# Kernel optimization log

Hardware: AMD Instinct MI355X
Metric: run time of the kernel (lower is better)

## Reference

```python
import jax, jax.numpy as jnp
import numpy as np

N_NODES = 100000
N_EDGES = 1600000
F_IN = 128
HID = 128
N_GRAPHS = 64


def setup_inputs() -> dict:
    key = jax.random.key(0)
    ks = jax.random.split(key, 12)
    x = jax.random.normal(ks[0], (N_NODES, F_IN), dtype=jnp.float32)
    edge_index = jax.random.randint(ks[1], (2, N_EDGES), 0, N_NODES, dtype=jnp.int32)
    batch = jnp.sort(jax.random.randint(ks[2], (N_NODES,), 0, N_GRAPHS, dtype=jnp.int32))
    s = 1.0 / np.sqrt(F_IN)
    W1 = jax.random.normal(ks[3], (F_IN, HID), dtype=jnp.float32) * s
    b1 = jnp.zeros((HID,), jnp.float32)
    W2 = jax.random.normal(ks[4], (HID, HID), dtype=jnp.float32) * s
    b2 = jnp.zeros((HID,), jnp.float32)
    W3 = jax.random.normal(ks[5], (HID, HID), dtype=jnp.float32) * s
    b3 = jnp.zeros((HID,), jnp.float32)
    Wc1 = jax.random.normal(ks[6], (HID, HID // 2), dtype=jnp.float32) * s
    bc1 = jnp.zeros((HID // 2,), jnp.float32)
    Wc2 = jax.random.normal(ks[7], (HID // 2, 1), dtype=jnp.float32) * (1.0 / np.sqrt(HID // 2))
    bc2 = jnp.zeros((1,), jnp.float32)
    return {"x": x, "edge_index": edge_index, "batch": batch,
            "W1": W1, "b1": b1, "W2": W2, "b2": b2, "W3": W3, "b3": b3,
            "Wc1": Wc1, "bc1": bc1, "Wc2": Wc2, "bc2": bc2}


def _gcn_conv(x, W, b, src, dst, norm, n_nodes):
    # PyG GCNConv: x' = D^-1/2 (A+I) D^-1/2 (x W) + b  (self-loops already in src/dst)
    h = x @ W                                   # [N, H] small GEMM
    msg = h[src] * norm[:, None]                # [E+N, H] gather (memory bound)
    out = jax.ops.segment_sum(msg, dst, num_segments=n_nodes)  # scatter-add
    return out + b


def reference(x, edge_index, batch, W1, b1, W2, b2, W3, b3, Wc1, bc1, Wc2, bc2):
    n = x.shape[0]
    loop = jnp.arange(n, dtype=edge_index.dtype)
    src = jnp.concatenate([edge_index[0], loop])
    dst = jnp.concatenate([edge_index[1], loop])
    deg = jax.ops.segment_sum(jnp.ones_like(dst, dtype=x.dtype), dst, num_segments=n)
    dinv = jax.lax.rsqrt(jnp.maximum(deg, 1.0))
    norm = dinv[src] * dinv[dst]                # [E+N]

    h = jax.nn.elu(_gcn_conv(x, W1, b1, src, dst, norm, n))   # dropout is identity in eval
    h = jax.nn.elu(_gcn_conv(h, W2, b2, src, dst, norm, n))
    h = jax.nn.elu(_gcn_conv(h, W3, b3, src, dst, norm, n))

    # global mean pool over graphs
    sums = jax.ops.segment_sum(h, batch, num_segments=N_GRAPHS)
    cnts = jax.ops.segment_sum(jnp.ones((n,), h.dtype), batch, num_segments=N_GRAPHS)
    g = sums / jnp.maximum(cnts, 1.0)[:, None]  # [G, H]

    z = jax.nn.relu(g @ Wc1 + bc1)
    logits = z @ Wc2 + bc2
    return jax.nn.sigmoid(logits)               # [G, 1]
```

## Files before the change

kernel.cpp:

```cpp
#include <hip/hip_runtime.h>
#include <cstdint>
#include <cstddef>


#define SUBCAP 512
#define CSRCAP 4608
#define TILE 4096

typedef __attribute__((ext_vector_type(8))) short short8;
typedef __attribute__((ext_vector_type(4))) float f32x4;
typedef __attribute__((ext_vector_type(2))) _Float16 h16x2;

__device__ __forceinline__ float bf2f(uint32_t u) {
  return __uint_as_float(u << 16);
}
__device__ __forceinline__ uint32_t f2bf(float f) {
  uint32_t x = __float_as_uint(f);
  return (x + 0x7FFFu + ((x >> 16) & 1u)) >> 16;
}

union H16 { _Float16 h; uint16_t u; };
union H2U { h16x2 h; uint32_t u; };

__device__ __forceinline__ uint32_t f2e5m2(float f) {
  f = fminf(fmaxf(f, -30000.f), 30000.f);
  H16 cv;
  cv.h = (_Float16)f;
  uint32_t h = cv.u;
  uint32_t r = h + 0x7Fu + ((h >> 8) & 1u);
  return (r >> 8) & 0xFFu;
}

__device__ __forceinline__ float e5m2f(uint32_t b) {
  H16 cv;
  cv.u = (uint16_t)(b << 8);
  return (float)cv.h;
}


__global__ __launch_bounds__(256) void bucket_scatter(const int* __restrict__ src,
                                                      const int* __restrict__ dst,
                                                      int* __restrict__ bcur,
                                                      uint32_t* __restrict__ ebuf,
                                                      int nE, int nbuk) {
  uint32_t xcc;
  asm("s_getreg_b32 %0, hwreg(HW_REG_XCC_ID)" : "=s"(xcc));
  __shared__ int lhist[1024];
  __shared__ int gbase[1024];
  int t = threadIdx.x;
  for (int i = t; i < nbuk; i += 256) lhist[i] = 0;
  __syncthreads();

  int e0 = blockIdx.x * TILE;
  int myd[16], mys[16], myrank[16];
#pragma unroll
  for (int j = 0; j < 16; ++j) {
    int e = e0 + t + j * 256;
    if (e < nE) {
      int d = dst[e];
      myd[j] = d;
      mys[j] = src[e];
      myrank[j] = atomicAdd(&lhist[d >> 7], 1);
    } else {
      myd[j] = -1;
    }
  }
  __syncthreads();
  for (int i = t; i < nbuk; i += 256) {
    int c = lhist[i];
    gbase[i] = c ? atomicAdd(&bcur[((i << 3) | (int)xcc) * 16], c) : 0;
  }
  __syncthreads();
#pragma unroll
  for (int j = 0; j < 16; ++j) {
    if (myd[j] >= 0) {
      int b = myd[j] >> 7;
      int pos = gbase[b] + myrank[j];
      if (pos < SUBCAP) {
        int sub = (b << 3) | (int)xcc;
        ebuf[(size_t)sub * SUBCAP + pos] =
            ((uint32_t)(myd[j] & 127) << 20) | (uint32_t)mys[j];
      }
    }
  }
}

__global__ __launch_bounds__(256) void bucket_build(const uint32_t* __restrict__ ebuf,
                                                    const int* __restrict__ bcur,
                                                    int* __restrict__ deg,
                                                    float* __restrict__ dinv,
                                                    int* __restrict__ offs,
                                                    int* __restrict__ csr,
                                                    const float* __restrict__ W1,
                                                    const float* __restrict__ W2,
                                                    const float* __restrict__ W3,
                                                    uint16_t* __restrict__ WT,
                                                    float* __restrict__ pool,
                                                    int n, int nbuk) {
  int b = blockIdx.x;
  int base = b << 7;
  __shared__ int hist[128];
  __shared__ int pre[128];
  __shared__ int lcur[128];
  int t = threadIdx.x;

  for (int id = b * 256 + t; id < 3 * 16384; id += nbuk * 256) {
    int w = id >> 14;
    int rem = id & 16383;
    int k = rem >> 7, nn = rem & 127;
    const float* W = (w == 0) ? W1 : ((w == 1) ? W2 : W3);
    WT[w * 16384 + nn * 128 + k] = (uint16_t)f2bf(W[k * 128 + nn]);
  }
  for (int id = b * 256 + t; id < 64 * 128; id += nbuk * 256) pool[id] = 0.f;

  if (t < 128) hist[t] = 0;
  __syncthreads();
  int cnts[8];
#pragma unroll
  for (int x = 0; x < 8; ++x) {
    int sub = (b << 3) | x;
    int cnt = min(bcur[sub * 16], SUBCAP);
    cnts[x] = cnt;
    const uint32_t* eb = ebuf + (size_t)sub * SUBCAP;
    for (int e = t; e < cnt; e += 256) atomicAdd(&hist[eb[e] >> 20], 1);
  }
  __syncthreads();
  if (t < 128) pre[t] = (hist[t] + 3) & ~3;
  __syncthreads();
  for (int d = 1; d < 128; d <<= 1) {
    int v = (t >= d && t < 128) ? pre[t - d] : 0;
    __syncthreads();
    if (t < 128) pre[t] += v;
    __syncthreads();
  }
  if (t < 128) {
    int dg = hist[t];
    int start = b * CSRCAP + pre[t] - ((dg + 3) & ~3);
    lcur[t] = start;
    if (base + t < n) {
      deg[base + t] = dg;
      dinv[base + t] = rsqrtf((float)(dg + 1));
      offs[base + t] = start;
    }
  }
  __syncthreads();
#pragma unroll
  for (int x = 0; x < 8; ++x) {
    int sub = (b << 3) | x;
    int cnt = cnts[x];
    const uint32_t* eb = ebuf + (size_t)sub * SUBCAP;
    for (int e = t; e < cnt; e += 256) {
      uint32_t ed = eb[e];
      int pos = atomicAdd(&lcur[ed >> 20], 1);
      csr[pos] = (int)((ed & 0xFFFFFu) << 7);
    }
  }
}


template <bool F32IN>
__global__ __launch_bounds__(256) void gemm_mfma(const uint16_t* __restrict__ Xb,
                                                 const float* __restrict__ X32,
                                                 const uint16_t* __restrict__ WTb,
                                                 const float* __restrict__ dinv,
                                                 uint8_t* __restrict__ tab, int n) {
  __shared__ uint16_t sW[128 * 136];
  int t = threadIdx.x;
#pragma unroll
  for (int i = 0; i < 8; ++i) {
    int j = t + i * 256;
    int r = j >> 4, c = j & 15;
    float4 v = ((const float4*)WTb)[j];
    *(float4*)(sW + r * 136 + c * 8) = v;
  }
  __syncthreads();

  int wave = t >> 6, lane = t & 63;
  int quad = lane >> 4, l15 = lane & 15;
  int m = blockIdx.x * 64 + wave * 16 + l15;
  int mm = min(m, n - 1);

  short8 a[4];
#pragma unroll
  for (int kc = 0; kc < 4; ++kc) {
    if constexpr (F32IN) {
      const float* p = X32 + (size_t)mm * 128 + kc * 32 + quad * 8;
      float4 lo = *(const float4*)p;
      float4 hi = *(const float4*)(p + 4);
      a[kc] = (short8){(short)f2bf(lo.x), (short)f2bf(lo.y),
                       (short)f2bf(lo.z), (short)f2bf(lo.w),
                       (short)f2bf(hi.x), (short)f2bf(hi.y),
                       (short)f2bf(hi.z), (short)f2bf(hi.w)};
    } else {
      a[kc] = *(const short8*)(Xb + (size_t)mm * 128 + kc * 32 + quad * 8);
    }
  }

  f32x4 acc[8];
#pragma unroll
  for (int nn = 0; nn < 8; ++nn) acc[nn] = (f32x4){0.f, 0.f, 0.f, 0.f};

#pragma unroll
  for (int nn = 0; nn < 8; ++nn) {
    int nrow = nn * 16 + l15;
#pragma unroll
    for (int kc = 0; kc < 4; ++kc) {
      short8 b = *(const short8*)(sW + nrow * 136 + kc * 32 + quad * 8);
      acc[nn] = __builtin_amdgcn_mfma_f32_16x16x32_bf16(a[kc], b, acc[nn], 0, 0, 0);
    }
  }

  int mrow = blockIdx.x * 64 + wave * 16 + quad * 4;
#pragma unroll
  for (int r = 0; r < 4; ++r) {
    int row = mrow + r;
    if (row < n) {
      float dn = dinv[row];
#pragma unroll
      for (int nn = 0; nn < 8; ++nn) {
        tab[(size_t)row * 128 + nn * 16 + l15] = (uint8_t)f2e5m2(acc[nn][r] * dn);
      }
    }
  }
}


__device__ __forceinline__ void acc_pk(uint32_t u, h16x2& a01, h16x2& a23) {
  H2U p01, p23;
  p01.u = __builtin_amdgcn_perm(u, 0u, 0x05010400u);
  p23.u = __builtin_amdgcn_perm(u, 0u, 0x07010600u);
  a01 += p01.h;
  a23 += p23.h;
}

__global__ __launch_bounds__(256) void gather_fused(const uint8_t* __restrict__ tab,
                                                    const int* __restrict__ csr,
                                                    const int* __restrict__ offs,
                                                    const int* __restrict__ deg,
                                                    const float* __restrict__ dinv,
                                                    const float* __restrict__ b,
                                                    uint16_t* __restrict__ out, int n) {
  int node = blockIdx.x * 8 + (threadIdx.x >> 5);
  if (node >= n) return;
  int l = threadIdx.x & 31;
  int c = l * 4;
  const uint8_t* tabc = tab + c;
  int e0 = offs[node];
  int e1 = e0 + deg[node];
  h16x2 a01 = (h16x2){(_Float16)0.f, (_Float16)0.f};
  h16x2 a23 = (h16x2){(_Float16)0.f, (_Float16)0.f};

  int e = e0;
  for (; e + 7 < e1; e += 8) {
    int4 ca = *(const int4*)(csr + e);
    int4 cb = *(const int4*)(csr + e + 4);
    uint32_t u[8];
    u[0] = *(const uint32_t*)(tabc + ca.x);
    u[1] = *(const uint32_t*)(tabc + ca.y);
    u[2] = *(const uint32_t*)(tabc + ca.z);
    u[3] = *(const uint32_t*)(tabc + ca.w);
    u[4] = *(const uint32_t*)(tabc + cb.x);
    u[5] = *(const uint32_t*)(tabc + cb.y);
    u[6] = *(const uint32_t*)(tabc + cb.z);
    u[7] = *(const uint32_t*)(tabc + cb.w);
#pragma unroll
    for (int j = 0; j < 8; ++j) acc_pk(u[j], a01, a23);
  }
  if (e + 3 < e1) {
    int4 ca = *(const int4*)(csr + e);
    uint32_t u[4];
    u[0] = *(const uint32_t*)(tabc + ca.x);
    u[1] = *(const uint32_t*)(tabc + ca.y);
    u[2] = *(const uint32_t*)(tabc + ca.z);
    u[3] = *(const uint32_t*)(tabc + ca.w);
#pragma unroll
    for (int j = 0; j < 4; ++j) acc_pk(u[j], a01, a23);
    e += 4;
  }
  for (; e < e1; ++e) acc_pk(*(const uint32_t*)(tabc + csr[e]), a01, a23);

  float a0 = (float)a01.x, a1 = (float)a01.y;
  float a2 = (float)a23.x, a3 = (float)a23.y;

  float dn = dinv[node];
  uint32_t uh = *(const uint32_t*)(tabc + node * 128);
  float4 bb = *(const float4*)(b + c);
  float o0 = (a0 + e5m2f(uh & 0xFFu)) * dn + bb.x;
  float o1 = (a1 + e5m2f((uh >> 8) & 0xFFu)) * dn + bb.y;
  float o2 = (a2 + e5m2f((uh >> 16) & 0xFFu)) * dn + bb.z;
  float o3 = (a3 + e5m2f(uh >> 24)) * dn + bb.w;
  o0 = o0 > 0.f ? o0 : expm1f(o0);
  o1 = o1 > 0.f ? o1 : expm1f(o1);
  o2 = o2 > 0.f ? o2 : expm1f(o2);
  o3 = o3 > 0.f ? o3 : expm1f(o3);
  uint2 po;
  po.x = f2bf(o0) | (f2bf(o1) << 16);
  po.y = f2bf(o2) | (f2bf(o3) << 16);
  *(uint2*)(out + (size_t)node * 128 + c) = po;
}


__global__ __launch_bounds__(128) void pool_kernel(const uint16_t* __restrict__ h,
                                                   const int* __restrict__ batch,
                                                   float* __restrict__ pool, int n) {
  int f = threadIdx.x;
  int i0 = blockIdx.x * 64;
  int iend = min(i0 + 64, n);
  __shared__ int sb[64];
  if (threadIdx.x < 64 && i0 + threadIdx.x < n) sb[threadIdx.x] = batch[i0 + threadIdx.x];
  __syncthreads();
  float acc = 0.f;
  int cur = sb[0];
  for (int i = i0; i < iend; ++i) {
    int g = sb[i - i0];
    if (g != cur) {
      atomicAdd(&pool[cur * 128 + f], acc);
      acc = 0.f;
      cur = g;
    }
    acc += bf2f((uint32_t)h[(size_t)i * 128 + f]);
  }
  atomicAdd(&pool[cur * 128 + f], acc);
}

__global__ __launch_bounds__(64) void classifier_kernel(const float* __restrict__ pool,
                                                        const int* __restrict__ batch,
                                                        const float* __restrict__ Wc1,
                                                        const float* __restrict__ bc1,
                                                        const float* __restrict__ Wc2,
                                                        const float* __restrict__ bc2,
                                                        float* __restrict__ out, int n) {
  int g = blockIdx.x;
  int j = threadIdx.x;
  __shared__ float sg[128];

  int lo = 0, hi = n;
  while (lo < hi) {
    int mid = (lo + hi) >> 1;
    if (batch[mid] < g) lo = mid + 1; else hi = mid;
  }
  int a = lo;
  lo = 0; hi = n;
  while (lo < hi) {
    int mid = (lo + hi) >> 1;
    if (batch[mid] < g + 1) lo = mid + 1; else hi = mid;
  }
  float inv = 1.f / (float)max(lo - a, 1);

  sg[j] = pool[g * 128 + j] * inv;
  sg[j + 64] = pool[g * 128 + j + 64] * inv;
  __syncthreads();

  float acc = bc1[j];
#pragma unroll 4
  for (int k = 0; k < 128; ++k) acc += sg[k] * Wc1[k * 64 + j];
  float z = fmaxf(acc, 0.f);

  float v = z * Wc2[j];
#pragma unroll
  for (int m = 32; m > 0; m >>= 1) v += __shfl_xor(v, m, 64);
  if (j == 0) out[g] = 1.f / (1.f + expf(-(v + bc2[0])));
}

extern "C" void kernel_launch(void* const* d_in, const int* in_sizes, int n_in,
                              void* d_out, int out_size, void* d_ws, size_t ws_size,
                              hipStream_t stream) {
  const float* x   = (const float*)d_in[0];
  const int* ei    = (const int*)d_in[1];
  const int* batch = (const int*)d_in[2];
  const float* W1  = (const float*)d_in[3];
  const float* b1  = (const float*)d_in[4];
  const float* W2  = (const float*)d_in[5];
  const float* b2  = (const float*)d_in[6];
  const float* W3  = (const float*)d_in[7];
  const float* b3  = (const float*)d_in[8];
  const float* Wc1 = (const float*)d_in[9];
  const float* bc1 = (const float*)d_in[10];
  const float* Wc2 = (const float*)d_in[11];
  const float* bc2 = (const float*)d_in[12];

  int n  = in_sizes[2];
  int nE = in_sizes[1] / 2;
  const int* src = ei;
  const int* dst = ei + nE;
  int nbuk = (n + 127) >> 7;

  uint8_t*  tab  = (uint8_t*)d_ws;
  uint16_t* bufO = (uint16_t*)(tab + (size_t)n * 128);
  float* dinv    = (float*)(bufO + (size_t)n * 128);
  int*   deg     = (int*)(dinv + n);
  int*   offs    = deg + n;
  int*   bcur    = offs + n + 4;
  int*   csr     = bcur + nbuk * 8 * 16;
  uint32_t* ebuf = (uint32_t*)(csr + (size_t)nbuk * CSRCAP);
  uint16_t* WT   = (uint16_t*)(ebuf + (size_t)nbuk * 8 * SUBCAP);
  float* pool    = (float*)(WT + 3 * 16384);
  float* out     = (float*)d_out;

  hipMemsetAsync(bcur, 0, (size_t)nbuk * 8 * 16 * sizeof(int), stream);
  bucket_scatter<<<(nE + TILE - 1) / TILE, 256, 0, stream>>>(src, dst, bcur, ebuf, nE, nbuk);
  bucket_build<<<nbuk, 256, 0, stream>>>(ebuf, bcur, deg, dinv, offs, csr,
                                         W1, W2, W3, WT, pool, n, nbuk);

  const float* bs[3] = {b1, b2, b3};
  for (int l = 0; l < 3; ++l) {
    if (l == 0)
      gemm_mfma<true><<<(n + 63) / 64, 256, 0, stream>>>(nullptr, x, WT, dinv, tab, n);
    else
      gemm_mfma<false><<<(n + 63) / 64, 256, 0, stream>>>(bufO, nullptr, WT + l * 16384, dinv, tab, n);
    gather_fused<<<(n + 7) / 8, 256, 0, stream>>>(tab, csr, offs, deg, dinv, bs[l], bufO, n);
  }

  pool_kernel<<<(n + 63) / 64, 128, 0, stream>>>(bufO, batch, pool, n);
  classifier_kernel<<<64, 64, 0, stream>>>(pool, batch, Wc1, bc1, Wc2, bc2, out, n);
}
```

Baseline: 350.3 us.

## Fuse gather with next layer GEMM and final mean-pool into one kernel

Each gather kernel now handles 16 nodes per 512-thread block. It stages the aggregated bf16 rows in shared memory and immediately multiplies them by the next layer's weight (loaded into LDS) with MFMA, writing the e5m2 table directly. The last layer instead does the graph pooling from shared memory, which removes the separate pool kernel and the bf16 intermediate round trips through global memory. Ping-pong tables replace the single tab/bufO pair. The cost is loading a 128x128 weight tile into LDS per 16-node block, plus higher LDS use that may reduce occupancy.

Result: faster. 336.3 us (-4.0%).

```diff
diff --git a/kernel.cpp b/kernel.cpp
--- a/kernel.cpp
+++ b/kernel.cpp
@@ -233,16 +233,39 @@
   a23 += p23.h;
 }
 
-__global__ __launch_bounds__(256) void gather_fused(const uint8_t* __restrict__ tab,
-                                                    const int* __restrict__ csr,
-                                                    const int* __restrict__ offs,
-                                                    const int* __restrict__ deg,
-                                                    const float* __restrict__ dinv,
-                                                    const float* __restrict__ b,
-                                                    uint16_t* __restrict__ out, int n) {
-  int node = blockIdx.x * 8 + (threadIdx.x >> 5);
-  if (node >= n) return;
-  int l = threadIdx.x & 31;
+template <bool POOL>
+__global__ __launch_bounds__(512) void gather_gemm(const uint8_t* __restrict__ tab,
+                                                   const int* __restrict__ csr,
+                                                   const int* __restrict__ offs,
+                                                   const int* __restrict__ deg,
+                                                   const float* __restrict__ dinv,
+                                                   const float* __restrict__ b,
+                                                   const uint16_t* __restrict__ WTb,
+                                                   uint8_t* __restrict__ tabN,
+                                                   const int* __restrict__ batch,
+                                                   float* __restrict__ pool,
+                                                   int n) {
+  __shared__ uint16_t sW[POOL ? 8 : 128 * 136];
+  __shared__ uint16_t sA[16 * 136];
+  __shared__ int sb[16];
+  int t = threadIdx.x;
+  int blk = (int)blockIdx.x;
+
+  if constexpr (!POOL) {
+#pragma unroll
+    for (int i = 0; i < 4; ++i) {
+      int j = t + i * 512;
+      int r = j >> 4, c = j & 15;
+      float4 v = ((const float4*)WTb)[j];
+      *(float4*)(sW + r * 136 + c * 8) = v;
+    }
+  } else {
+    if (t < 16) sb[t] = batch[min(blk * 16 + t, n - 1)];
+  }
+
+  int hw = t >> 5;
+  int node = min(blk * 16 + hw, n - 1);
+  int l = t & 31;
   int c = l * 4;
   const uint8_t* tabc = tab + c;
   int e0 = offs[node];
@@ -296,32 +319,48 @@
   uint2 po;
   po.x = f2bf(o0) | (f2bf(o1) << 16);
   po.y = f2bf(o2) | (f2bf(o3) << 16);
-  *(uint2*)(out + (size_t)node * 128 + c) = po;
-}
-
-
-__global__ __launch_bounds__(128) void pool_kernel(const uint16_t* __restrict__ h,
-                                                   const int* __restrict__ batch,
-                                                   float* __restrict__ pool, int n) {
-  int f = threadIdx.x;
-  int i0 = blockIdx.x * 64;
-  int iend = min(i0 + 64, n);
-  __shared__ int sb[64];
-  if (threadIdx.x < 64 && i0 + threadIdx.x < n) sb[threadIdx.x] = batch[i0 + threadIdx.x];
-  __syncthreads();
-  float acc = 0.f;
-  int cur = sb[0];
-  for (int i = i0; i < iend; ++i) {
-    int g = sb[i - i0];
-    if (g != cur) {
-      atomicAdd(&pool[cur * 128 + f], acc);
-      acc = 0.f;
-      cur = g;
-    }
-    acc += bf2f((uint32_t)h[(size_t)i * 128 + f]);
-  }
-  atomicAdd(&pool[cur * 128 + f], acc);
-}
+  *(uint2*)(sA + hw * 136 + c) = po;
+  __syncthreads();
+
+  if constexpr (POOL) {
+    if (t < 128) {
+      int base = blk * 16;
+      int iend = min(16, n - base);
+      float acc = 0.f;
+      int cur = sb[0];
+      for (int i = 0; i < iend; ++i) {
+        int g = sb[i];
+        if (g != cur) {
+          atomicAdd(&pool[cur * 128 + t], acc);
+          acc = 0.f;
+          cur = g;
+        }
+        acc += bf2f((uint32_t)sA[i * 136 + t]);
+      }
+      atomicAdd(&pool[cur * 128 + t], acc);
+    }
+  } else {
+    int wave = t >> 6, lane = t & 63;
+    int quad = lane >> 4, l15 = lane & 15;
+    f32x4 acc = (f32x4){0.f, 0.f, 0.f, 0.f};
+#pragma unroll
+    for (int kc = 0; kc < 4; ++kc) {
+      short8 av = *(const short8*)(sA + l15 * 136 + kc * 32 + quad * 8);
+      short8 bv = *(const short8*)(sW + (wave * 16 + l15) * 136 + kc * 32 + quad * 8);
+      acc = __builtin_amdgcn_mfma_f32_16x16x32_bf16(av, bv, acc, 0, 0, 0);
+    }
+    int mrow = blk * 16 + quad * 4;
+#pragma unroll
+    for (int r = 0; r < 4; ++r) {
+      int row = mrow + r;
+      if (row < n) {
+        float dno = dinv[row];
+        tabN[(size_t)row * 128 + wave * 16 + l15] = (uint8_t)f2e5m2(acc[r] * dno);
+      }
+    }
+  }
+}
+
 
 __global__ __launch_bounds__(64) void classifier_kernel(const float* __restrict__ pool,
                                                         const int* __restrict__ batch,
@@ -385,9 +424,9 @@
   const int* dst = ei + nE;
   int nbuk = (n + 127) >> 7;
 
-  uint8_t*  tab  = (uint8_t*)d_ws;
-  uint16_t* bufO = (uint16_t*)(tab + (size_t)n * 128);
-  float* dinv    = (float*)(bufO + (size_t)n * 128);
+  uint8_t*  tab0 = (uint8_t*)d_ws;
+  uint8_t*  tab1 = tab0 + (size_t)n * 128;
+  float* dinv    = (float*)(tab0 + (size_t)n * 128 + (size_t)n * 256);
   int*   deg     = (int*)(dinv + n);
   int*   offs    = deg + n;
   int*   bcur    = offs + n + 4;
@@ -402,15 +441,13 @@
   bucket_build<<<nbuk, 256, 0, stream>>>(ebuf, bcur, deg, dinv, offs, csr,
                                          W1, W2, W3, WT, pool, n, nbuk);
 
-  const float* bs[3] = {b1, b2, b3};
-  for (int l = 0; l < 3; ++l) {
-    if (l == 0)
-      gemm_mfma<true><<<(n + 63) / 64, 256, 0, stream>>>(nullptr, x, WT, dinv, tab, n);
-    else
-      gemm_mfma<false><<<(n + 63) / 64, 256, 0, stream>>>(bufO, nullptr, WT + l * 16384, dinv, tab, n);
-    gather_fused<<<(n + 7) / 8, 256, 0, stream>>>(tab, csr, offs, deg, dinv, bs[l], bufO, n);
-  }
-
-  pool_kernel<<<(n + 63) / 64, 128, 0, stream>>>(bufO, batch, pool, n);
+  int gfb = (n + 15) / 16;
+  gemm_mfma<true><<<(n + 63) / 64, 256, 0, stream>>>(nullptr, x, WT, dinv, tab0, n);
+  gather_gemm<false><<<gfb, 512, 0, stream>>>(tab0, csr, offs, deg, dinv, b1,
+                                              WT + 16384, tab1, nullptr, nullptr, n);
+  gather_gemm<false><<<gfb, 512, 0, stream>>>(tab1, csr, offs, deg, dinv, b2,
+                                              WT + 32768, tab0, nullptr, nullptr, n);
+  gather_gemm<true><<<gfb, 512, 0, stream>>>(tab0, csr, offs, deg, dinv, b3,
+                                             nullptr, nullptr, batch, pool, n);
   classifier_kernel<<<64, 64, 0, stream>>>(pool, batch, Wc1, bc1, Wc2, bc2, out, n);
 }
```
